# Kernel optimization log

Measured on AMD Instinct MI355X. Metric: run time of the kernel, lower is better.

## Reference

```python
import jax, jax.numpy as jnp
import numpy as np

NBATCH, NUMATOM, NEIGH = 16, 512, 48
NPAIR = NUMATOM * NEIGH
NTYPE, NWAVE, NIPSIN = 4, 8, 3
CUTOFF = 5.0  # note: cutoff_cosine is never applied in the original forward


def setup_inputs() -> dict:
    key = jax.random.key(0)
    k1, k2, k3, k4 = jax.random.split(key, 4)
    coordinates = jax.random.normal(k1, (NBATCH, NUMATOM, 3), jnp.float32) * 3.0
    numatoms = jnp.full((NBATCH, 1), NUMATOM, dtype=jnp.int32)  # unused by forward math
    atom_index = jax.random.randint(k2, (NBATCH, 2, NPAIR), 0, NUMATOM)
    shifts = jax.random.normal(k3, (NBATCH, NPAIR, 3), jnp.float32)  # all > -1e9 -> all pairs valid
    species = jax.random.randint(k4, (NBATCH * NUMATOM,), 0, NTYPE)
    rs = jnp.tile(jnp.linspace(0.5, 4.0, NWAVE, dtype=jnp.float32), (NTYPE, 1))
    inta = jnp.full((NTYPE, NWAVE), 0.1, dtype=jnp.float32)
    return {"coordinates": coordinates, "numatoms": numatoms, "atom_index": atom_index,
            "shifts": shifts, "species": species, "rs": rs, "inta": inta}


def _forward(coordinates, atom_index, shifts, species, rs, inta):
    nbatch, numatom, _ = coordinates.shape
    totnatom = nbatch * numatom
    npair = atom_index.shape[2]
    coords = coordinates.reshape(-1, 3)                      # (totnatom, 3)
    # (nbatch, 2, P) -> (2, nbatch*P) with per-molecule global offsets
    ai = atom_index.transpose(1, 0, 2).reshape(2, -1)
    offs = jnp.repeat(jnp.arange(nbatch) * numatom, npair)
    idx12 = ai + offs[None, :]
    sh = shifts.reshape(-1, 3)
    valid = jnp.all(sh > -1e9, axis=1)                       # padding mask (all True here)
    dist_vec = coords[idx12[0]] - coords[idx12[1]] + sh      # (N, 3)
    distances = jnp.linalg.norm(dist_vec, axis=-1)           # (N,)
    neigh_sp = species[idx12[0]]                             # (N,)
    # radial: exp(-10*inta_t*(r - rs_t)^2), species-gathered params
    g = jnp.exp(-10.0 * inta[neigh_sp] * jnp.square(distances[:, None] - rs[neigh_sp]))  # (N, nwave)
    # angular: repeated outer products of the unit direction vector
    u = (dist_vec / distances[:, None]).T                    # (3, N)
    parts, orb = [], jnp.ones((1, u.shape[1]), u.dtype)
    for _ in range(1, NIPSIN):
        orb = jnp.einsum('jn,kn->jkn', orb, u).reshape(-1, u.shape[1])
        parts.append(orb)
    angular = jnp.concatenate(parts, axis=0)                 # (len_index=12, N)
    index_para = jnp.concatenate([jnp.full((3 ** i,), i - 1, dtype=jnp.int32)
                                  for i in range(1, NIPSIN)])
    # outer product of angular and radial basis per pair
    oa = jnp.einsum('jn,nk->njk', angular, g)                # (N, len_index, nwave)
    density_cols = []
    for itype in range(NTYPE):
        m = ((neigh_sp == itype) & valid).astype(oa.dtype)
        pd = jax.ops.segment_sum(oa * m[:, None, None], idx12[0], num_segments=totnatom)
        pd = jnp.square(pd)                                  # (totnatom, len_index, nwave)
        # sum angular components of equal order (index_para); row NIPSIN-1 stays zero, as in torch
        idens = jax.ops.segment_sum(pd.transpose(1, 0, 2), index_para, num_segments=NIPSIN)
        density_cols.append(idens.transpose(1, 0, 2).reshape(totnatom, -1))
    density = jnp.stack(density_cols, axis=1)                # (totnatom, ntype, nipsin*nwave)
    return density.reshape(totnatom, -1)


def reference(coordinates, numatoms, atom_index, shifts, species, rs, inta):
    return _forward(coordinates, atom_index, shifts, species, rs, inta)
```

## Files before the change

kernel.cpp:

```cpp
#include <hip/hip_runtime.h>

#define NBATCH   16
#define NUMATOM  512
#define NEIGH    48
#define NPAIR    (NUMATOM * NEIGH)
#define TOT_PAIR (NBATCH * NPAIR)
#define TOTNATOM (NBATCH * NUMATOM)
#define NTYPE    4
#define NWAVE    8
#define NIPSIN   3
#define NROWS    9
#define CAP      96
#define OUT_PER_ATOM (NTYPE * NIPSIN * NWAVE)

#define SC_BLOCK 512
#define PAIRS_PER_BLOCK 1024
#define BLOCKS_PER_BATCH (NPAIR / PAIRS_PER_BLOCK)

__global__ __launch_bounds__(SC_BLOCK, 2) void scatter_pairs(
        const float* __restrict__ coords,
        const int*   __restrict__ atom_index,
        const float* __restrict__ shifts,
        int*         __restrict__ cnt,
        float4*      __restrict__ pd) {
    __shared__ float lc[NUMATOM * 3];

    int blk   = blockIdx.x;
    int b     = blk / BLOCKS_PER_BATCH;
    int pbase = (blk - b * BLOCKS_PER_BATCH) * PAIRS_PER_BLOCK;

    const float* cb = coords + (size_t)b * NUMATOM * 3;
    for (int t = threadIdx.x; t < NUMATOM * 3; t += SC_BLOCK) lc[t] = cb[t];
    __syncthreads();

    const int*   i0row = atom_index + ((size_t)b * 2 + 0) * NPAIR + pbase;
    const int*   i1row = atom_index + ((size_t)b * 2 + 1) * NPAIR + pbase;
    const float* shrow = shifts + ((size_t)b * NPAIR + pbase) * 3;

    int t = threadIdx.x;
#pragma unroll
    for (int k = 0; k < 2; ++k) {
        int p  = t + k * SC_BLOCK;
        int a0 = i0row[p];
        int a1 = i1row[p];
        float sx = shrow[3 * p + 0];
        float sy = shrow[3 * p + 1];
        float sz = shrow[3 * p + 2];

        float dx = lc[3 * a0 + 0] - lc[3 * a1 + 0] + sx;
        float dy = lc[3 * a0 + 1] - lc[3 * a1 + 1] + sy;
        float dz = lc[3 * a0 + 2] - lc[3 * a1 + 2] + sz;

        float r   = sqrtf(dx * dx + dy * dy + dz * dz);
        float inv = 1.0f / r;

        int gi0  = b * NUMATOM + a0;
        int slot = atomicAdd(&cnt[gi0], 1);
        if (slot < CAP)
            pd[(size_t)gi0 * CAP + slot] =
                make_float4(dx * inv, dy * inv, dz * inv, r);
    }
}

__global__ __launch_bounds__(64, 8) void gather_density(
        const float4* __restrict__ pd,
        const int*    __restrict__ cnt,
        const int*    __restrict__ species,
        const float*  __restrict__ rs,
        const float*  __restrict__ inta,
        float*        __restrict__ out) {
    __shared__ float4 lp[CAP];
    __shared__ float  qsh[NROWS * NWAVE];
    __shared__ float  ord[2][NWAVE];

    int a  = blockIdx.x;
    int l  = threadIdx.x;
    int sp = species[a];
    int c  = cnt[a];
    if (c > CAP) c = CAP;

    for (int p = l; p < c; p += 64) lp[p] = pd[(size_t)a * CAP + p];
    __syncthreads();

    int j = l >> 3, w = l & 7;
    float rw = rs[sp * NWAVE + w];
    float cw = -10.0f * inta[sp * NWAVE + w];

    int ia, ib;
    if (j < 3)      { ia = j;     ib = 3;     }
    else if (j < 6) { ia = j - 3; ib = j - 3; }
    else if (j == 6){ ia = 0;     ib = 1;     }
    else            { ia = 0;     ib = 2;     }

    float acc = 0.0f, acc2 = 0.0f;
    int p = 0;
    for (; p + 2 <= c; p += 2) {
        float4 v0 = lp[p];
        float4 v1 = lp[p + 1];
        float d0 = v0.w - rw, d1 = v1.w - rw;
        float g0 = __expf(cw * d0 * d0);
        float g1 = __expf(cw * d1 * d1);
        float ua0 = (ia == 0) ? v0.x : (ia == 1) ? v0.y : v0.z;
        float ub0 = (ib == 0) ? v0.x : (ib == 1) ? v0.y : (ib == 2) ? v0.z : 1.0f;
        float ua1 = (ia == 0) ? v1.x : (ia == 1) ? v1.y : v1.z;
        float ub1 = (ib == 0) ? v1.x : (ib == 1) ? v1.y : (ib == 2) ? v1.z : 1.0f;
        acc  += ua0 * ub0 * g0 + ua1 * ub1 * g1;
        acc2 += v0.y * v0.z * g0 + v1.y * v1.z * g1;
    }
    for (; p < c; ++p) {
        float4 v = lp[p];
        float d = v.w - rw;
        float g = __expf(cw * d * d);
        float ua = (ia == 0) ? v.x : (ia == 1) ? v.y : v.z;
        float ub = (ib == 0) ? v.x : (ib == 1) ? v.y : (ib == 2) ? v.z : 1.0f;
        acc  += ua * ub * g;
        acc2 += v.y * v.z * g;
    }

    qsh[l] = acc * acc;
    if (l < 8) qsh[64 + l] = acc2 * acc2;
    __syncthreads();

    if (l < 8) {
        int w0 = l;
        ord[0][w0] = qsh[w0] + qsh[8 + w0] + qsh[16 + w0];
        ord[1][w0] = qsh[24 + w0] + qsh[32 + w0] + qsh[40 + w0]
                   + 2.0f * (qsh[48 + w0] + qsh[56 + w0] + qsh[64 + w0]);
    }
    __syncthreads();

    float* ob = out + (size_t)a * OUT_PER_ATOM;
    for (int o = l; o < OUT_PER_ATOM; o += 64) {
        int ity = o / 24;
        int rem = o - ity * 24;
        int od  = rem >> 3;
        int ww  = rem & 7;
        ob[o] = (ity == sp && od < 2) ? ord[od][ww] : 0.0f;
    }
}


extern "C" void kernel_launch(void* const* d_in, const int* in_sizes, int n_in,
                              void* d_out, int out_size, void* d_ws, size_t ws_size,
                              hipStream_t stream) {
    const float* coords     = (const float*)d_in[0];
    const int*   atom_index = (const int*)  d_in[2];
    const float* shifts     = (const float*)d_in[3];
    const int*   species    = (const int*)  d_in[4];
    const float* rs         = (const float*)d_in[5];
    const float* inta       = (const float*)d_in[6];
    float*       out        = (float*)      d_out;

    const size_t cnt_bytes = (size_t)TOTNATOM * sizeof(int);
    const size_t pd_off    = (cnt_bytes + 255) & ~(size_t)255;
    int*    cnt = (int*)d_ws;
    float4* pd  = (float4*)((char*)d_ws + pd_off);

    hipMemsetAsync(cnt, 0, cnt_bytes, stream);

    scatter_pairs<<<NBATCH * BLOCKS_PER_BATCH, SC_BLOCK, 0, stream>>>(
        coords, atom_index, shifts, cnt, pd);
    gather_density<<<TOTNATOM, 64, 0, stream>>>(pd, cnt, species, rs, inta, out);
}
```

Baseline: 102.9 us.

## Accumulate per-atom density in LDS partials, then reduce across chunks

```diff
diff --git a/kernel.cpp b/kernel.cpp
--- a/kernel.cpp
+++ b/kernel.cpp
@@ -4,138 +4,149 @@
 #define NUMATOM  512
 #define NEIGH    48
 #define NPAIR    (NUMATOM * NEIGH)
-#define TOT_PAIR (NBATCH * NPAIR)
 #define TOTNATOM (NBATCH * NUMATOM)
 #define NTYPE    4
 #define NWAVE    8
-#define NIPSIN   3
-#define NROWS    9
-#define CAP      96
-#define OUT_PER_ATOM (NTYPE * NIPSIN * NWAVE)
+#define OUT_PER_ATOM 96
 
-#define SC_BLOCK 512
-#define PAIRS_PER_BLOCK 1024
-#define BLOCKS_PER_BATCH (NPAIR / PAIRS_PER_BLOCK)
+#define NQ      4
+#define NC      8
+#define RATOMS  (NUMATOM / NQ)
+#define CHUNK   (NPAIR / NC)
+#define ASTRIDE 73
+#define QCAP    1024
+#define PLANE   (RATOMS * 72)
 
-__global__ __launch_bounds__(SC_BLOCK, 2) void scatter_pairs(
+__global__ __launch_bounds__(256, 2) void partial_accum(
         const float* __restrict__ coords,
         const int*   __restrict__ atom_index,
         const float* __restrict__ shifts,
-        int*         __restrict__ cnt,
-        float4*      __restrict__ pd) {
+        const int*   __restrict__ species,
+        const float* __restrict__ rs,
+        const float* __restrict__ inta,
+        float*       __restrict__ part) {
+    __shared__ float acc[RATOMS * ASTRIDE];
     __shared__ float lc[NUMATOM * 3];
+    __shared__ int   lsp[RATOMS];
+    __shared__ float lrs[NTYPE * NWAVE];
+    __shared__ float lia[NTYPE * NWAVE];
+    __shared__ int   queue[QCAP];
+    __shared__ int   qn;
 
-    int blk   = blockIdx.x;
-    int b     = blk / BLOCKS_PER_BATCH;
-    int pbase = (blk - b * BLOCKS_PER_BATCH) * PAIRS_PER_BLOCK;
+    int blk = blockIdx.x;
+    int c   = blk % NC;
+    int q   = (blk / NC) % NQ;
+    int b   = blk / (NC * NQ);
+    int t   = threadIdx.x;
+    int lo  = q * RATOMS;
 
+    for (int i = t; i < RATOMS * ASTRIDE; i += 256) acc[i] = 0.0f;
     const float* cb = coords + (size_t)b * NUMATOM * 3;
-    for (int t = threadIdx.x; t < NUMATOM * 3; t += SC_BLOCK) lc[t] = cb[t];
+    for (int i = t; i < NUMATOM * 3; i += 256) lc[i] = cb[i];
+    if (t < RATOMS) lsp[t] = species[b * NUMATOM + lo + t];
+    if (t < NTYPE * NWAVE) { lrs[t] = rs[t]; lia[t] = -10.0f * inta[t]; }
+    if (t == 0) qn = 0;
     __syncthreads();
 
-    const int*   i0row = atom_index + ((size_t)b * 2 + 0) * NPAIR + pbase;
-    const int*   i1row = atom_index + ((size_t)b * 2 + 1) * NPAIR + pbase;
-    const float* shrow = shifts + ((size_t)b * NPAIR + pbase) * 3;
+    const int* i0row = atom_index + ((size_t)b * 2 + 0) * NPAIR + (size_t)c * CHUNK;
+    for (int i = t; i < CHUNK; i += 256) {
+        int a0 = i0row[i];
+        if ((a0 >> 7) == q) {
+            int slot = atomicAdd(&qn, 1);
+            if (slot < QCAP) queue[slot] = i | ((a0 & (RATOMS - 1)) << 16);
+        }
+    }
+    __syncthreads();
+    int nkeep = qn < QCAP ? qn : QCAP;
 
-    int t = threadIdx.x;
-#pragma unroll
-    for (int k = 0; k < 2; ++k) {
-        int p  = t + k * SC_BLOCK;
-        int a0 = i0row[p];
+    const int*   i1row = atom_index + ((size_t)b * 2 + 1) * NPAIR + (size_t)c * CHUNK;
+    const float* shrow = shifts + ((size_t)b * NPAIR + (size_t)c * CHUNK) * 3;
+
+    for (int i = t; i < nkeep; i += 256) {
+        int e  = queue[i];
+        int p  = e & 0xFFFF;
+        int al = e >> 16;
+        int a0 = lo + al;
         int a1 = i1row[p];
-        float sx = shrow[3 * p + 0];
-        float sy = shrow[3 * p + 1];
-        float sz = shrow[3 * p + 2];
 
-        float dx = lc[3 * a0 + 0] - lc[3 * a1 + 0] + sx;
-        float dy = lc[3 * a0 + 1] - lc[3 * a1 + 1] + sy;
-        float dz = lc[3 * a0 + 2] - lc[3 * a1 + 2] + sz;
+        float dx = lc[3 * a0 + 0] - lc[3 * a1 + 0] + shrow[3 * p + 0];
+        float dy = lc[3 * a0 + 1] - lc[3 * a1 + 1] + shrow[3 * p + 1];
+        float dz = lc[3 * a0 + 2] - lc[3 * a1 + 2] + shrow[3 * p + 2];
 
         float r   = sqrtf(dx * dx + dy * dy + dz * dz);
         float inv = 1.0f / r;
+        float ux = dx * inv, uy = dy * inv, uz = dz * inv;
 
-        int gi0  = b * NUMATOM + a0;
-        int slot = atomicAdd(&cnt[gi0], 1);
-        if (slot < CAP)
-            pd[(size_t)gi0 * CAP + slot] =
-                make_float4(dx * inv, dy * inv, dz * inv, r);
-    }
-}
+        int sp = lsp[al];
+        float g[NWAVE];
+#pragma unroll
+        for (int w = 0; w < NWAVE; ++w) {
+            float d = r - lrs[sp * NWAVE + w];
+            g[w] = __expf(lia[sp * NWAVE + w] * d * d);
+        }
+        float ang[9] = { ux, uy, uz,
+                         ux * ux, uy * uy, uz * uz,
+                         ux * uy, ux * uz, uy * uz };
 
-__global__ __launch_bounds__(64, 8) void gather_density(
-        const float4* __restrict__ pd,
-        const int*    __restrict__ cnt,
-        const int*    __restrict__ species,
-        const float*  __restrict__ rs,
-        const float*  __restrict__ inta,
-        float*        __restrict__ out) {
-    __shared__ float4 lp[CAP];
-    __shared__ float  qsh[NROWS * NWAVE];
-    __shared__ float  ord[2][NWAVE];
-
-    int a  = blockIdx.x;
-    int l  = threadIdx.x;
-    int sp = species[a];
-    int c  = cnt[a];
-    if (c > CAP) c = CAP;
-
-    for (int p = l; p < c; p += 64) lp[p] = pd[(size_t)a * CAP + p];
-    __syncthreads();
-
-    int j = l >> 3, w = l & 7;
-    float rw = rs[sp * NWAVE + w];
-    float cw = -10.0f * inta[sp * NWAVE + w];
-
-    int ia, ib;
-    if (j < 3)      { ia = j;     ib = 3;     }
-    else if (j < 6) { ia = j - 3; ib = j - 3; }
-    else if (j == 6){ ia = 0;     ib = 1;     }
-    else            { ia = 0;     ib = 2;     }
-
-    float acc = 0.0f, acc2 = 0.0f;
-    int p = 0;
-    for (; p + 2 <= c; p += 2) {
-        float4 v0 = lp[p];
-        float4 v1 = lp[p + 1];
-        float d0 = v0.w - rw, d1 = v1.w - rw;
-        float g0 = __expf(cw * d0 * d0);
-        float g1 = __expf(cw * d1 * d1);
-        float ua0 = (ia == 0) ? v0.x : (ia == 1) ? v0.y : v0.z;
-        float ub0 = (ib == 0) ? v0.x : (ib == 1) ? v0.y : (ib == 2) ? v0.z : 1.0f;
-        float ua1 = (ia == 0) ? v1.x : (ia == 1) ? v1.y : v1.z;
-        float ub1 = (ib == 0) ? v1.x : (ib == 1) ? v1.y : (ib == 2) ? v1.z : 1.0f;
-        acc  += ua0 * ub0 * g0 + ua1 * ub1 * g1;
-        acc2 += v0.y * v0.z * g0 + v1.y * v1.z * g1;
-    }
-    for (; p < c; ++p) {
-        float4 v = lp[p];
-        float d = v.w - rw;
-        float g = __expf(cw * d * d);
-        float ua = (ia == 0) ? v.x : (ia == 1) ? v.y : v.z;
-        float ub = (ib == 0) ? v.x : (ib == 1) ? v.y : (ib == 2) ? v.z : 1.0f;
-        acc  += ua * ub * g;
-        acc2 += v.y * v.z * g;
-    }
-
-    qsh[l] = acc * acc;
-    if (l < 8) qsh[64 + l] = acc2 * acc2;
-    __syncthreads();
-
-    if (l < 8) {
-        int w0 = l;
-        ord[0][w0] = qsh[w0] + qsh[8 + w0] + qsh[16 + w0];
-        ord[1][w0] = qsh[24 + w0] + qsh[32 + w0] + qsh[40 + w0]
-                   + 2.0f * (qsh[48 + w0] + qsh[56 + w0] + qsh[64 + w0]);
+        float* ab = acc + al * ASTRIDE;
+#pragma unroll
+        for (int j = 0; j < 9; ++j)
+#pragma unroll
+            for (int w = 0; w < NWAVE; ++w)
+                atomicAdd(&ab[j * NWAVE + w], ang[j] * g[w]);
     }
     __syncthreads();
 
+    float* pb = part + (size_t)blk * PLANE;
+    for (int i = t; i < PLANE; i += 256)
+        pb[i] = acc[(i / 72) * ASTRIDE + (i % 72)];
+}
+
+__global__ __launch_bounds__(256) void reduce_finalize(
+        const float* __restrict__ part,
+        const int*   __restrict__ species,
+        float*       __restrict__ out) {
+    int wv = threadIdx.x >> 6;
+    int l  = threadIdx.x & 63;
+    int a  = blockIdx.x * 4 + wv;
+
+    int b   = a >> 9;
+    int al  = a & (NUMATOM - 1);
+    int q   = al >> 7;
+    int arl = al & (RATOMS - 1);
+
+    size_t base = ((size_t)(b * NQ + q) * NC) * PLANE + (size_t)arl * 72;
+
+    float val = 0.0f, val2 = 0.0f;
+#pragma unroll
+    for (int c = 0; c < NC; ++c) {
+        const float* pl = part + base + (size_t)c * PLANE;
+        val += pl[l];
+        if (l < 8) val2 += pl[64 + l];
+    }
+
+    float dens = val * val;
+    int j = l >> 3;
+    float A = (j < 3) ? dens : 0.0f;
+    float B = (j >= 3 && j < 6) ? dens
+            : (j >= 6) ? 2.0f * dens : 0.0f;
+    if (l < 8) B = 2.0f * val2 * val2;
+
+#pragma unroll
+    for (int m = 8; m < 64; m <<= 1) {
+        A += __shfl_xor(A, m);
+        B += __shfl_xor(B, m);
+    }
+
+    int sp = species[a];
     float* ob = out + (size_t)a * OUT_PER_ATOM;
-    for (int o = l; o < OUT_PER_ATOM; o += 64) {
-        int ity = o / 24;
-        int rem = o - ity * 24;
-        int od  = rem >> 3;
-        int ww  = rem & 7;
-        ob[o] = (ity == sp && od < 2) ? ord[od][ww] : 0.0f;
+    {
+        int o = l, ity = o / 24, rem = o % 24, od = rem >> 3;
+        ob[o] = (ity == sp && od < 2) ? (od == 0 ? A : B) : 0.0f;
+    }
+    if (l < 32) {
+        int o = l + 64, ity = o / 24, rem = o % 24, od = rem >> 3;
+        ob[o] = (ity == sp && od < 2) ? (od == 0 ? A : B) : 0.0f;
     }
 }
 
@@ -150,15 +161,9 @@
     const float* rs         = (const float*)d_in[5];
     const float* inta       = (const float*)d_in[6];
     float*       out        = (float*)      d_out;
+    float*       part       = (float*)      d_ws;
 
-    const size_t cnt_bytes = (size_t)TOTNATOM * sizeof(int);
-    const size_t pd_off    = (cnt_bytes + 255) & ~(size_t)255;
-    int*    cnt = (int*)d_ws;
-    float4* pd  = (float4*)((char*)d_ws + pd_off);
-
-    hipMemsetAsync(cnt, 0, cnt_bytes, stream);
-
-    scatter_pairs<<<NBATCH * BLOCKS_PER_BATCH, SC_BLOCK, 0, stream>>>(
-        coords, atom_index, shifts, cnt, pd);
-    gather_density<<<TOTNATOM, 64, 0, stream>>>(pd, cnt, species, rs, inta, out);
+    partial_accum<<<NBATCH * NQ * NC, 256, 0, stream>>>(
+        coords, atom_index, shifts, species, rs, inta, part);
+    reduce_finalize<<<TOTNATOM / 4, 256, 0, stream>>>(part, species, out);
 }
```

New measurement: 238.8 us. 2.32x slower.
